# Kernel optimization log

Hardware: AMD Instinct MI355X
Metric: run time of the kernel (lower is better)

Reference implementation:

```python
import jax, jax.numpy as jnp
import numpy as np

B = 8192  # number of covariance matrices
N = 64    # n_assets


def setup_inputs() -> dict:
    key = jax.random.key(0)
    A = jax.random.normal(key, (B, N, N), dtype=jnp.float32)
    # SPD covariance: A A^T / N + 0.1 I  (real covariances are SPD)
    sigma = jnp.einsum('bij,bkj->bik', A, A) / N + 0.1 * jnp.eye(N, dtype=jnp.float32)
    return {"sigma": sigma}


def reference(sigma) -> jnp.ndarray:
    # Symmetrize, as the original does: 0.5 * (S + S^T)
    sym = 0.5 * (sigma + jnp.swapaxes(sigma, -1, -2))  # [B, N, N]
    n = sym.shape[-1]
    ones = jnp.ones((*sym.shape[:-2], n), dtype=sym.dtype)  # [B, N]
    # Closed-form min-variance (short selling allowed): w = S^-1 1 / (1^T S^-1 1)
    z = jnp.linalg.solve(sym, ones[..., None])[..., 0]      # [B, N]
    w = z / jnp.sum(z, axis=-1, keepdims=True)              # [B, N]
    return w[..., None]  # [B, N, 1], matching expand_dims(axis=-1)
```

## Files before the change

### kernel.cpp

```cpp
#include <hip/hip_runtime.h>


#define NN 64

typedef float v2f __attribute__((ext_vector_type(2)));

template <int I> struct ic { static constexpr int value = I; };

template <int Start, int End, typename F>
__device__ __forceinline__ void static_for(F&& f) {
    if constexpr (Start < End) {
        f(ic<Start>{});
        static_for<Start + 1, End>(static_cast<F&&>(f));
    }
}

__device__ __forceinline__ float rlane(float v, int lane) {
    return __int_as_float(__builtin_amdgcn_readlane(__float_as_int(v), lane));
}

__device__ __forceinline__ float frcp(float x) {
#if __has_builtin(__builtin_amdgcn_rcpf)
    return __builtin_amdgcn_rcpf(x);
#else
    return 1.0f / x;
#endif
}

__device__ __forceinline__ v2f fma2(v2f a, v2f b, v2f c) {
#if __has_builtin(__builtin_elementwise_fma)
    return __builtin_elementwise_fma(a, b, c);
#else
    v2f r; r.x = fmaf(a.x, b.x, c.x); r.y = fmaf(a.y, b.y, c.y); return r;
#endif
}

__global__ __launch_bounds__(256)
__attribute__((amdgpu_waves_per_eu(2, 4)))
void minvar_kernel(const float* __restrict__ sigma,
                   float* __restrict__ out,
                   int batch) {
    const int lane = threadIdx.x & 63;
    const int wid  = threadIdx.x >> 6;
    const int bid  = blockIdx.x * 4 + wid;
    if (bid >= batch) return;

    const float* __restrict__ p = sigma + (size_t)bid * (NN * NN) + (size_t)lane * NN;

    v2f r[NN / 2];
    static_for<0, NN / 4>([&](auto j4c) {
        constexpr int j4 = decltype(j4c)::value;
        float4 v = reinterpret_cast<const float4*>(p)[j4];
        r[2 * j4 + 0] = v2f{v.x, v.y};
        r[2 * j4 + 1] = v2f{v.z, v.w};
    });

    float b = 1.0f;

    static_for<0, NN>([&](auto kc) {
        constexpr int k  = decltype(kc)::value;
        constexpr int pk = k / 2;
        const float ekk  = (k & 1) ? r[pk].y : r[pk].x;
        const float pivot = rlane(ekk, k);
        const float invp  = frcp(pivot);
        const float nf    = (lane > k) ? (-ekk * invp) : 0.0f;
        const v2f   nf2   = v2f{nf, nf};
        b = fmaf(nf, rlane(b, k), b);

        if constexpr ((k & 1) == 0) {
            const float bcy = rlane(r[pk].y, k);
            r[pk].y = fmaf(nf, bcy, r[pk].y);
        }

        constexpr int P0 = pk + 1;
        static_for<0, (NN / 2 - P0 + 3) / 4>([&](auto gc) {
            constexpr int g0 = P0 + 4 * decltype(gc)::value;
            v2f bc[4];
            static_for<0, 4>([&](auto tc) {
                constexpr int t = decltype(tc)::value;
                if constexpr (g0 + t < NN / 2)
                    bc[t] = v2f{rlane(r[g0 + t].x, k), rlane(r[g0 + t].y, k)};
            });
            static_for<0, 4>([&](auto tc) {
                constexpr int t = decltype(tc)::value;
                if constexpr (g0 + t < NN / 2)
                    r[g0 + t] = fma2(nf2, bc[t], r[g0 + t]);
            });
        });
    });

    static_for<0, NN>([&](auto kk) {
        constexpr int k  = NN - 1 - decltype(kk)::value;
        constexpr int pk = k / 2;
        const float ekk  = (k & 1) ? r[pk].y : r[pk].x;
        const float ukk  = rlane(ekk, k);
        const float yk   = rlane(b, k);
        const float zk   = yk * frcp(ukk);
        const float upd  = (lane < k) ? (-ekk) : 0.0f;
        b = (lane == k) ? zk : fmaf(upd, zk, b);
    });

    float total = b;
    #pragma unroll
    for (int off = 32; off >= 1; off >>= 1)
        total += __shfl_xor(total, off, 64);

    out[(size_t)bid * NN + lane] = b * frcp(total);
}

extern "C" void kernel_launch(void* const* d_in, const int* in_sizes, int n_in,
                              void* d_out, int out_size, void* d_ws, size_t ws_size,
                              hipStream_t stream) {
    const float* sigma = (const float*)d_in[0];
    float* out = (float*)d_out;
    const int batch = in_sizes[0] / (NN * NN);
    const int blocks = (batch + 3) / 4;
    minvar_kernel<<<blocks, 256, 0, stream>>>(sigma, out, batch);
}
```

Before: 204.9 us.

## Split each matrix across two waves with Gauss-Jordan elimination via LDS

Each 64x64 system is now handled by two wavefronts, each owning alternating columns (32 registers instead of 64). Elimination factors are exchanged through shared memory with a block barrier every pivot step. Forward elimination becomes full Gauss-Jordan, which removes the back-substitution loop. Lower register use is meant to raise occupancy (waves_per_eu 6-8) and hide latency, at the cost of 64 __syncthreads per matrix, redundant b updates in both waves, and LDS traffic.

```diff
diff --git a/kernel.cpp b/kernel.cpp
--- a/kernel.cpp
+++ b/kernel.cpp
@@ -36,76 +36,96 @@
 }
 
 __global__ __launch_bounds__(256)
-__attribute__((amdgpu_waves_per_eu(2, 4)))
+__attribute__((amdgpu_waves_per_eu(6, 8)))
 void minvar_kernel(const float* __restrict__ sigma,
                    float* __restrict__ out,
                    int batch) {
+    __shared__ float nf_buf[2][NN];
+    __shared__ float dg_buf[2][NN];
+
     const int lane = threadIdx.x & 63;
     const int wid  = threadIdx.x >> 6;
-    const int bid  = blockIdx.x * 4 + wid;
-    if (bid >= batch) return;
+    const int mloc = wid >> 1;
+    const int h    = wid & 1;
+    int bid = blockIdx.x * 2 + mloc;
+    if (bid >= batch) bid = batch - 1;
 
-    const float* __restrict__ p = sigma + (size_t)bid * (NN * NN) + (size_t)lane * NN;
+    const float* __restrict__ rowp =
+        sigma + (size_t)bid * (NN * NN) + (size_t)lane * NN + h;
 
-    v2f r[NN / 2];
-    static_for<0, NN / 4>([&](auto j4c) {
-        constexpr int j4 = decltype(j4c)::value;
-        float4 v = reinterpret_cast<const float4*>(p)[j4];
-        r[2 * j4 + 0] = v2f{v.x, v.y};
-        r[2 * j4 + 1] = v2f{v.z, v.w};
+    float r[NN / 2];
+    static_for<0, NN / 2>([&](auto mc) {
+        constexpr int m = decltype(mc)::value;
+        r[m] = rowp[2 * m];
     });
 
     float b = 1.0f;
+    float d = 0.0f;
+    float* __restrict__ nfp = &nf_buf[mloc][0];
+    float* __restrict__ dgp = &dg_buf[mloc][0];
 
     static_for<0, NN>([&](auto kc) {
         constexpr int k  = decltype(kc)::value;
-        constexpr int pk = k / 2;
-        const float ekk  = (k & 1) ? r[pk].y : r[pk].x;
-        const float pivot = rlane(ekk, k);
-        const float invp  = frcp(pivot);
-        const float nf    = (lane > k) ? (-ekk * invp) : 0.0f;
-        const v2f   nf2   = v2f{nf, nf};
+        constexpr int kp = k & 1;
+        constexpr int m0 = k >> 1;
+
+        float nf;
+        if (h == kp) {
+            const float aik   = r[m0];
+            const float pivot = rlane(aik, k);
+            d  = (lane == k) ? pivot : d;
+            nf = (lane != k) ? (-aik * frcp(pivot)) : 0.0f;
+            nfp[lane] = nf;
+        }
+        __syncthreads();
+        if (h != kp) nf = nfp[lane];
+
         b = fmaf(nf, rlane(b, k), b);
 
-        if constexpr ((k & 1) == 0) {
-            const float bcy = rlane(r[pk].y, k);
-            r[pk].y = fmaf(nf, bcy, r[pk].y);
+        if constexpr (kp == 0) {
+            const float g = (h != 0) ? nf : 0.0f;
+            r[m0] = fmaf(g, rlane(r[m0], k), r[m0]);
         }
 
-        constexpr int P0 = pk + 1;
-        static_for<0, (NN / 2 - P0 + 3) / 4>([&](auto gc) {
-            constexpr int g0 = P0 + 4 * decltype(gc)::value;
+        constexpr int F   = m0 + 1;
+        constexpr int cnt = (NN / 2) - F;
+        constexpr int F2  = F + (cnt & 1);
+        if constexpr (cnt & 1)
+            r[F] = fmaf(nf, rlane(r[F], k), r[F]);
+
+        const v2f nf2 = v2f{nf, nf};
+        static_for<0, (NN / 2 - F2 + 7) / 8>([&](auto gc) {
+            constexpr int g0 = F2 + 8 * decltype(gc)::value;
             v2f bc[4];
             static_for<0, 4>([&](auto tc) {
                 constexpr int t = decltype(tc)::value;
-                if constexpr (g0 + t < NN / 2)
-                    bc[t] = v2f{rlane(r[g0 + t].x, k), rlane(r[g0 + t].y, k)};
+                if constexpr (g0 + 2 * t + 1 < NN / 2)
+                    bc[t] = v2f{rlane(r[g0 + 2 * t], k),
+                                rlane(r[g0 + 2 * t + 1], k)};
             });
             static_for<0, 4>([&](auto tc) {
                 constexpr int t = decltype(tc)::value;
-                if constexpr (g0 + t < NN / 2)
-                    r[g0 + t] = fma2(nf2, bc[t], r[g0 + t]);
+                if constexpr (g0 + 2 * t + 1 < NN / 2) {
+                    v2f cur = v2f{r[g0 + 2 * t], r[g0 + 2 * t + 1]};
+                    cur = fma2(nf2, bc[t], cur);
+                    r[g0 + 2 * t]     = cur.x;
+                    r[g0 + 2 * t + 1] = cur.y;
+                }
             });
         });
     });
 
-    static_for<0, NN>([&](auto kk) {
-        constexpr int k  = NN - 1 - decltype(kk)::value;
-        constexpr int pk = k / 2;
-        const float ekk  = (k & 1) ? r[pk].y : r[pk].x;
-        const float ukk  = rlane(ekk, k);
-        const float yk   = rlane(b, k);
-        const float zk   = yk * frcp(ukk);
-        const float upd  = (lane < k) ? (-ekk) : 0.0f;
-        b = (lane == k) ? zk : fmaf(upd, zk, b);
-    });
+    if ((lane & 1) == h) dgp[lane] = d;
+    __syncthreads();
+    const float z = b * frcp(dgp[lane]);
 
-    float total = b;
+    float tot = z;
     #pragma unroll
     for (int off = 32; off >= 1; off >>= 1)
-        total += __shfl_xor(total, off, 64);
+        tot += __shfl_xor(tot, off, 64);
 
-    out[(size_t)bid * NN + lane] = b * frcp(total);
+    if (h == 0)
+        out[(size_t)bid * NN + lane] = z * frcp(tot);
 }
 
 extern "C" void kernel_launch(void* const* d_in, const int* in_sizes, int n_in,
@@ -113,7 +133,7 @@
                               hipStream_t stream) {
     const float* sigma = (const float*)d_in[0];
     float* out = (float*)d_out;
-    const int batch = in_sizes[0] / (NN * NN);
-    const int blocks = (batch + 3) / 4;
+    const int batch  = in_sizes[0] / (NN * NN);
+    const int blocks = (batch + 1) / 2;
     minvar_kernel<<<blocks, 256, 0, stream>>>(sigma, out, batch);
 }
```

After: 217.6 us. 6.2% more time.
